# Optimization experiments

Measured on AMD Instinct MI355X. Metric: run time of the kernel, lower is better.

## Reference

```python
import jax, jax.numpy as jnp
import numpy as np

HEADS = 16
LN_EPS = 1e-5

def _ln(v, w, b):
    # LayerNorm over last dim (head dim s)
    mu = jnp.mean(v, axis=-1, keepdims=True)
    var = jnp.mean(jnp.square(v - mu), axis=-1, keepdims=True)
    return (v - mu) * jax.lax.rsqrt(var + LN_EPS) * w + b

def setup_inputs() -> dict:
    key = jax.random.key(0)
    ks = jax.random.split(key, 5)
    b, t, e = 2, 2048, 1024
    x = jax.random.normal(ks[0], (b, t, e), dtype=jnp.float32)
    scale = 0.02
    Wk = jax.random.normal(ks[1], (e, e), dtype=jnp.float32) * scale
    Wq = jax.random.normal(ks[2], (e, e), dtype=jnp.float32) * scale
    Wv = jax.random.normal(ks[3], (e, e), dtype=jnp.float32) * scale
    Wu = jax.random.normal(ks[4], (e, e), dtype=jnp.float32) * scale
    s = e // HEADS
    return {
        "x": x, "Wk": Wk, "Wq": Wq, "Wv": Wv, "Wu": Wu,
        "kln_w": jnp.ones((s,), jnp.float32), "kln_b": jnp.zeros((s,), jnp.float32),
        "qln_w": jnp.ones((s,), jnp.float32), "qln_b": jnp.zeros((s,), jnp.float32),
    }

def reference(x, Wk, Wq, Wv, Wu, kln_w, kln_b, qln_w, qln_b):
    b, t, e = x.shape
    h = HEADS
    s = e // h
    # nn.Linear: y = x @ W^T
    k = (x @ Wk.T).reshape(b, t, h, s)
    q = (x @ Wq.T).reshape(b, t, h, s)
    v = (x @ Wv.T).reshape(b, t, h, s)
    k = _ln(k, kln_w, kln_b)
    q = _ln(q, qln_w, qln_b)
    scalefactor = 1.0 / np.sqrt(s).astype(np.float32)
    # [b, h, t_q, t_k]
    dot = jnp.einsum('bqhs,bkhs->bhqk', q, k) * scalefactor
    causal = jnp.triu(jnp.ones((t, t), dtype=bool), k=1)  # mask strictly-upper (diag kept)
    dot = jnp.where(causal, -jnp.inf, dot)
    attn = jax.nn.softmax(dot, axis=-1)
    out = jnp.einsum('bhqk,bkhs->bqhs', attn, v).reshape(b, t, e)
    return out @ Wu.T
```

## Files before the change

### kernel.cpp

```cpp
#include <hip/hip_runtime.h>
#include <math.h>

#define T_SEQ 2048
#define E_DIM 1024
#define NH    16
#define HS    64
#define NB    2
#define M_ROWS 4096

typedef __attribute__((ext_vector_type(8))) short bf16x8;
typedef __attribute__((ext_vector_type(4))) short bf16x4;
typedef __attribute__((ext_vector_type(4))) float f32x4;

#define AS1 __attribute__((address_space(1)))
#define AS3 __attribute__((address_space(3)))

#define LOG2E 1.4426950408889634f

__device__ __forceinline__ f32x4 mfma16(bf16x4 a, bf16x4 b, f32x4 c) {
    return __builtin_amdgcn_mfma_f32_16x16x16bf16_1k(a, b, c, 0, 0, 0);
}

__device__ __forceinline__ ushort f2bf(float f) {
    union { float f; unsigned u; } c; c.f = f;
    unsigned r = c.u + 0x7fffu + ((c.u >> 16) & 1u);
    return (ushort)(r >> 16);
}
__device__ __forceinline__ ushort f2bf_trunc(float f) {
    union { float f; unsigned u; } c; c.f = f;
    return (ushort)(c.u >> 16);
}

__device__ __forceinline__ void load_lds16(const ushort* g, ushort* l) {
    __builtin_amdgcn_global_load_lds((const AS1 unsigned int*)g,
                                     (AS3 unsigned int*)l, 16, 0, 0);
}

__global__ __launch_bounds__(256) void cvt_all(
    const float* __restrict__ x,  const float* __restrict__ Wk,
    const float* __restrict__ Wq, const float* __restrict__ Wv,
    const float* __restrict__ Wu,
    ushort* __restrict__ xb,  ushort* __restrict__ Wkb,
    ushort* __restrict__ Wqb, ushort* __restrict__ Wvb,
    ushort* __restrict__ Wub)
{
    int i4 = blockIdx.x * 256 + threadIdx.x;
    int region = i4 >> 18;
    const float* src; ushort* dst; int off;
    if      (region < 4)  { src = x;  dst = xb;  off = i4; }
    else if (region == 4) { src = Wk; dst = Wkb; off = i4 - (4 << 18); }
    else if (region == 5) { src = Wq; dst = Wqb; off = i4 - (5 << 18); }
    else if (region == 6) { src = Wv; dst = Wvb; off = i4 - (6 << 18); }
    else                  { src = Wu; dst = Wub; off = i4 - (7 << 18); }
    float4 v = *(const float4*)(src + (size_t)off * 4);
    ushort4 o; o.x = f2bf(v.x); o.y = f2bf(v.y); o.z = f2bf(v.z); o.w = f2bf(v.w);
    *(ushort4*)(dst + (size_t)off * 4) = o;
}

__device__ __forceinline__ void gemm_core(
    const ushort* __restrict__ A, const ushort* __restrict__ W,
    int m0, int n0, ushort* As, ushort* Bs, f32x4 acc[4][4])
{
    const int tid  = threadIdx.x;
    const int lane = tid & 63, w = tid >> 6;
    const int quad = lane >> 4, l16 = lane & 15;
    const int wm = w & 1, wn = w >> 1;

    const int rl   = lane >> 2;
    const int gsw  = (lane & 3) ^ ((lane >> 3) & 3);
    const int fsw  = (l16 >> 1) & 3;

    const f32x4 zero = {0.f, 0.f, 0.f, 0.f};
#pragma unroll
    for (int mt = 0; mt < 4; ++mt)
#pragma unroll
        for (int nt = 0; nt < 4; ++nt) acc[mt][nt] = zero;

    for (int k0 = 0; k0 < E_DIM; k0 += 32) {
#pragma unroll
        for (int i = 0; i < 2; ++i) {
            int c = i * 4 + w;
            int row = c * 16 + rl;
            load_lds16(A + (size_t)(m0 + row) * E_DIM + k0 + gsw * 8, As + c * 512);
            load_lds16(W + (size_t)(n0 + row) * E_DIM + k0 + gsw * 8, Bs + c * 512);
        }
        __syncthreads();
        bf16x8 af[4], bfr[4];
#pragma unroll
        for (int mt = 0; mt < 4; ++mt)
            af[mt] = *(const bf16x8*)(As + (wm * 64 + mt * 16 + l16) * 32
                                      + ((quad ^ fsw) * 8));
#pragma unroll
        for (int nt = 0; nt < 4; ++nt)
            bfr[nt] = *(const bf16x8*)(Bs + (wn * 64 + nt * 16 + l16) * 32
                                       + ((quad ^ fsw) * 8));
#pragma unroll
        for (int mt = 0; mt < 4; ++mt)
#pragma unroll
            for (int nt = 0; nt < 4; ++nt)
                acc[mt][nt] = __builtin_amdgcn_mfma_f32_16x16x32_bf16(
                    af[mt], bfr[nt], acc[mt][nt], 0, 0, 0);
        __syncthreads();
    }
}

__global__ __launch_bounds__(256) void gemm_qkv(
    const ushort* __restrict__ A,
    const ushort* __restrict__ W0, const ushort* __restrict__ W1,
    const ushort* __restrict__ W2,
    ushort* __restrict__ Kb, ushort* __restrict__ Qb, ushort* __restrict__ Vt,
    const float* __restrict__ kw, const float* __restrict__ kbias,
    const float* __restrict__ qw, const float* __restrict__ qbias)
{
    __shared__ ushort As[128 * 32];
    __shared__ ushort Bs[128 * 32];
    const int z = blockIdx.z;
    const ushort* W = (z == 0) ? W0 : (z == 1) ? W1 : W2;
    const int m0 = blockIdx.y * 128, n0 = blockIdx.x * 128;
    f32x4 acc[4][4];
    gemm_core(A, W, m0, n0, As, Bs, acc);

    const int lane = threadIdx.x & 63, w = threadIdx.x >> 6;
    const int quad = lane >> 4, l16 = lane & 15;
    const int wm = w & 1, wn = w >> 1;
    const int row0 = m0 + wm * 64;
    const int col0 = n0 + wn * 64;

    if (z < 2) {
        ushort* C = z ? Qb : Kb;
        const float* lw = z ? qw : kw;
        const float* lb = z ? qbias : kbias;
        const float scale = z ? (0.125f * LOG2E) : 1.0f;
        float wv[4], bv_[4];
#pragma unroll
        for (int nt = 0; nt < 4; ++nt) {
            wv[nt]  = lw[nt * 16 + l16];
            bv_[nt] = lb[nt * 16 + l16];
        }
#pragma unroll
        for (int mt = 0; mt < 4; ++mt)
#pragma unroll
            for (int r = 0; r < 4; ++r) {
                float v[4], d[4];
#pragma unroll
                for (int nt = 0; nt < 4; ++nt) v[nt] = acc[mt][nt][r];
                float s = v[0] + v[1] + v[2] + v[3];
                s += __shfl_xor(s, 1); s += __shfl_xor(s, 2);
                s += __shfl_xor(s, 4); s += __shfl_xor(s, 8);
                float mu = s * (1.0f / 64.0f);
                float q2 = 0.f;
#pragma unroll
                for (int nt = 0; nt < 4; ++nt) { d[nt] = v[nt] - mu; q2 += d[nt] * d[nt]; }
                q2 += __shfl_xor(q2, 1); q2 += __shfl_xor(q2, 2);
                q2 += __shfl_xor(q2, 4); q2 += __shfl_xor(q2, 8);
                float rin = rsqrtf(q2 * (1.0f / 64.0f) + 1e-5f);
                int row = row0 + mt * 16 + quad * 4 + r;
#pragma unroll
                for (int nt = 0; nt < 4; ++nt)
                    C[(size_t)row * E_DIM + col0 + nt * 16 + l16] =
                        f2bf((d[nt] * rin * wv[nt] + bv_[nt]) * scale);
            }
    } else {
        const int bidx = m0 >> 11;
        const int hh   = col0 >> 6;
        const int t0   = (m0 & 2047) + wm * 64;
#pragma unroll
        for (int mt = 0; mt < 4; ++mt)
#pragma unroll
            for (int nt = 0; nt < 4; ++nt) {
                ushort4 pk = make_ushort4(f2bf(acc[mt][nt][0]), f2bf(acc[mt][nt][1]),
                                          f2bf(acc[mt][nt][2]), f2bf(acc[mt][nt][3]));
                size_t off = ((size_t)(bidx * NH + hh) * 64 + nt * 16 + l16) * T_SEQ
                             + t0 + mt * 16 + quad * 4;
                *(ushort4*)(Vt + off) = pk;
            }
    }
}

__global__ __launch_bounds__(256) void gemm_o(
    const ushort* __restrict__ A, const ushort* __restrict__ W,
    float* __restrict__ C)
{
    __shared__ ushort As[128 * 32];
    __shared__ ushort Bs[64 * 32];
    const int tid  = threadIdx.x;
    const int lane = tid & 63, w = tid >> 6;
    const int quad = lane >> 4, l16 = lane & 15;
    const int wm = w & 1, wn = w >> 1;
    const int m0 = blockIdx.y * 128, n0 = blockIdx.x * 64;

    const int rl  = lane >> 2;
    const int gsw = (lane & 3) ^ ((lane >> 3) & 3);
    const int fsw = (l16 >> 1) & 3;

    const f32x4 zero = {0.f, 0.f, 0.f, 0.f};
    f32x4 acc[4][2];
#pragma unroll
    for (int mt = 0; mt < 4; ++mt)
#pragma unroll
        for (int nt = 0; nt < 2; ++nt) acc[mt][nt] = zero;

    for (int k0 = 0; k0 < E_DIM; k0 += 32) {
#pragma unroll
        for (int i = 0; i < 2; ++i) {
            int c = i * 4 + w;
            int row = c * 16 + rl;
            load_lds16(A + (size_t)(m0 + row) * E_DIM + k0 + gsw * 8, As + c * 512);
        }
        {
            int row = w * 16 + rl;
            load_lds16(W + (size_t)(n0 + row) * E_DIM + k0 + gsw * 8, Bs + w * 512);
        }
        __syncthreads();
        bf16x8 af[4], bfr[2];
#pragma unroll
        for (int mt = 0; mt < 4; ++mt)
            af[mt] = *(const bf16x8*)(As + (wm * 64 + mt * 16 + l16) * 32
                                      + ((quad ^ fsw) * 8));
#pragma unroll
        for (int nt = 0; nt < 2; ++nt)
            bfr[nt] = *(const bf16x8*)(Bs + (wn * 32 + nt * 16 + l16) * 32
                                       + ((quad ^ fsw) * 8));
#pragma unroll
        for (int mt = 0; mt < 4; ++mt)
#pragma unroll
            for (int nt = 0; nt < 2; ++nt)
                acc[mt][nt] = __builtin_amdgcn_mfma_f32_16x16x32_bf16(
                    af[mt], bfr[nt], acc[mt][nt], 0, 0, 0);
        __syncthreads();
    }

    const int row0 = m0 + wm * 64;
    const int col0 = n0 + wn * 32;
#pragma unroll
    for (int mt = 0; mt < 4; ++mt)
#pragma unroll
        for (int nt = 0; nt < 2; ++nt)
#pragma unroll
            for (int r = 0; r < 4; ++r)
                C[(size_t)(row0 + mt * 16 + quad * 4 + r) * E_DIM
                  + col0 + nt * 16 + l16] = acc[mt][nt][r];
}

__global__ __launch_bounds__(256, 4) void flash_attn5(
    const ushort* __restrict__ Qg, const ushort* __restrict__ Kg,
    const ushort* __restrict__ Vt, ushort* __restrict__ O)
{
    __shared__ ushort Ks[2][64 * 64];
    __shared__ ushort Vs[2][64 * 64];

    const int tid  = threadIdx.x;
    const int lane = tid & 63, w = tid >> 6;
    const int quad = lane >> 4, l16 = lane & 15;

    const int L = blockIdx.x;
    const int c = L & 255, s = L >> 8;
    const int q0 = c >> 5;
    const int bh = c & 31;
    const int qt = (s == 0) ? q0 : (s == 1) ? (15 - q0)
                 : (s == 2) ? (16 + q0) : (31 - q0);
    const int b = bh >> 4, h = bh & 15;

    const ushort* Qbase = Qg + ((size_t)b * T_SEQ) * E_DIM + h * HS;
    const ushort* Kbase = Kg + ((size_t)b * T_SEQ) * E_DIM + h * HS;
    const ushort* Vbase = Vt + ((size_t)bh * HS) * T_SEQ;

    const int rloc = lane >> 3;
    const int gswc = (lane & 7) ^ rloc;
    const int sw   = l16 & 7;

    bf16x8 aq[2];
#pragma unroll
    for (int ks = 0; ks < 2; ++ks)
        aq[ks] = *(const bf16x8*)(Qbase + (size_t)(qt * 64 + w * 16 + l16) * E_DIM
                                  + ks * 32 + quad * 8);

    const f32x4 zero = {0.f, 0.f, 0.f, 0.f};
    f32x4 o_acc[4];
#pragma unroll
    for (int dt = 0; dt < 4; ++dt) o_acc[dt] = zero;
    float l_acc = 0.f;

#pragma unroll
    for (int i = 0; i < 2; ++i) {
        int cc = w * 2 + i, row = cc * 8 + rloc;
        load_lds16(Kbase + (size_t)row * E_DIM + gswc * 8, Ks[0] + cc * 512);
        load_lds16(Vbase + (size_t)row * T_SEQ + gswc * 8, Vs[0] + cc * 512);
    }

    const float M8 = 8.0f * LOG2E;

    for (int jt = 0; jt <= qt; ++jt) {
        const int buf = jt & 1;
        __syncthreads();
        if (jt < qt) {
#pragma unroll
            for (int i = 0; i < 2; ++i) {
                int cc = w * 2 + i, row = cc * 8 + rloc;
                load_lds16(Kbase + (size_t)(jt + 1) * 64 * E_DIM
                           + (size_t)row * E_DIM + gswc * 8, Ks[buf ^ 1] + cc * 512);
                load_lds16(Vbase + (size_t)row * T_SEQ + (jt + 1) * 64 + gswc * 8,
                           Vs[buf ^ 1] + cc * 512);
            }
        }

        f32x4 sa[4];
#pragma unroll
        for (int nt = 0; nt < 4; ++nt) sa[nt] = zero;
#pragma unroll
        for (int ks = 0; ks < 2; ++ks) {
            int cp = ((ks * 4 + quad) ^ sw) * 8;
#pragma unroll
            for (int nt = 0; nt < 4; ++nt) {
                bf16x8 bk = *(const bf16x8*)(Ks[buf] + (nt * 16 + l16) * 64 + cp);
                sa[nt] = __builtin_amdgcn_mfma_f32_16x16x32_bf16(bk, aq[ks], sa[nt], 0, 0, 0);
            }
        }

        if (jt == qt) {
#pragma unroll
            for (int nt = 0; nt < 4; ++nt)
#pragma unroll
                for (int r = 0; r < 4; ++r)
                    if (nt * 16 + quad * 4 + r > w * 16 + l16) sa[nt][r] = -1e30f;
        }

        bf16x4 bp[4];
#pragma unroll
        for (int nt = 0; nt < 4; ++nt)
#pragma unroll
            for (int r = 0; r < 4; ++r) {
                float p = __builtin_amdgcn_exp2f(sa[nt][r] - M8);
                l_acc += p;
                bp[nt][r] = (short)f2bf_trunc(p);
            }

#pragma unroll
        for (int kt = 0; kt < 4; ++kt) {
            const int tt = kt * 16 + quad * 4;
            const int ch = tt >> 3, el = tt & 7;
#pragma unroll
            for (int dt = 0; dt < 4; ++dt) {
                const int vd = dt * 16 + l16;
                bf16x4 va = *(const bf16x4*)(Vs[buf] + vd * 64
                                             + ((ch ^ (vd & 7)) << 3) + el);
                o_acc[dt] = mfma16(va, bp[kt], o_acc[dt]);
            }
        }
    }

    l_acc += __shfl_xor(l_acc, 16);
    l_acc += __shfl_xor(l_acc, 32);
    const float inv = 1.0f / l_acc;
    const int trow = qt * 64 + w * 16 + l16;
#pragma unroll
    for (int dt = 0; dt < 4; ++dt) {
        ushort4 pk = make_ushort4(f2bf(o_acc[dt][0] * inv), f2bf(o_acc[dt][1] * inv),
                                  f2bf(o_acc[dt][2] * inv), f2bf(o_acc[dt][3] * inv));
        *(ushort4*)(O + ((size_t)b * T_SEQ + trow) * E_DIM + h * HS
                    + dt * 16 + quad * 4) = pk;
    }
}

extern "C" void kernel_launch(void* const* d_in, const int* in_sizes, int n_in,
                              void* d_out, int out_size, void* d_ws, size_t ws_size,
                              hipStream_t stream) {
    const float* x     = (const float*)d_in[0];
    const float* Wk    = (const float*)d_in[1];
    const float* Wq    = (const float*)d_in[2];
    const float* Wv    = (const float*)d_in[3];
    const float* Wu    = (const float*)d_in[4];
    const float* kln_w = (const float*)d_in[5];
    const float* kln_b = (const float*)d_in[6];
    const float* qln_w = (const float*)d_in[7];
    const float* qln_b = (const float*)d_in[8];
    float* out = (float*)d_out;

    const size_t NE = (size_t)M_ROWS * E_DIM;
    const size_t NW = (size_t)E_DIM * E_DIM;
    ushort* xb  = (ushort*)d_ws;
    ushort* Wkb = xb  + NE;
    ushort* Wqb = Wkb + NW;
    ushort* Wvb = Wqb + NW;
    ushort* Wub = Wvb + NW;
    ushort* Kb  = Wub + NW;
    ushort* Qb  = Kb  + NE;
    ushort* Vt  = Qb  + NE;
    ushort* Ob  = Vt  + NE;

    cvt_all<<<8192, 256, 0, stream>>>(x, Wk, Wq, Wv, Wu, xb, Wkb, Wqb, Wvb, Wub);

    gemm_qkv<<<dim3(E_DIM / 128, M_ROWS / 128, 3), 256, 0, stream>>>(
        xb, Wkb, Wqb, Wvb, Kb, Qb, Vt, kln_w, kln_b, qln_w, qln_b);

    flash_attn5<<<1024, 256, 0, stream>>>(Qb, Kb, Vt, Ob);

    gemm_o<<<dim3(E_DIM / 64, M_ROWS / 128), 256, 0, stream>>>(Ob, Wub, out);
}
```

Before: 181.9 us.

## Double-buffer LDS tiles in GEMMs and enlarge output projection tiles

```diff
diff --git a/kernel.cpp b/kernel.cpp
--- a/kernel.cpp
+++ b/kernel.cpp
@@ -57,7 +57,7 @@
     *(ushort4*)(dst + (size_t)off * 4) = o;
 }
 
-__device__ __forceinline__ void gemm_core(
+__device__ __forceinline__ void gemm_core_db(
     const ushort* __restrict__ A, const ushort* __restrict__ W,
     int m0, int n0, ushort* As, ushort* Bs, f32x4 acc[4][4])
 {
@@ -76,23 +76,40 @@
 #pragma unroll
         for (int nt = 0; nt < 4; ++nt) acc[mt][nt] = zero;
 
+#pragma unroll
+    for (int i = 0; i < 2; ++i) {
+        int c = i * 4 + w;
+        int row = c * 16 + rl;
+        load_lds16(A + (size_t)(m0 + row) * E_DIM + gsw * 8, As + c * 512);
+        load_lds16(W + (size_t)(n0 + row) * E_DIM + gsw * 8, Bs + c * 512);
+    }
+
     for (int k0 = 0; k0 < E_DIM; k0 += 32) {
-#pragma unroll
-        for (int i = 0; i < 2; ++i) {
-            int c = i * 4 + w;
-            int row = c * 16 + rl;
-            load_lds16(A + (size_t)(m0 + row) * E_DIM + k0 + gsw * 8, As + c * 512);
-            load_lds16(W + (size_t)(n0 + row) * E_DIM + k0 + gsw * 8, Bs + c * 512);
-        }
+        const int buf = (k0 >> 5) & 1;
+        ushort* Ab = As + buf * 4096;
+        ushort* Bb = Bs + buf * 4096;
         __syncthreads();
+        if (k0 + 32 < E_DIM) {
+            ushort* An = As + (buf ^ 1) * 4096;
+            ushort* Bn = Bs + (buf ^ 1) * 4096;
+#pragma unroll
+            for (int i = 0; i < 2; ++i) {
+                int c = i * 4 + w;
+                int row = c * 16 + rl;
+                load_lds16(A + (size_t)(m0 + row) * E_DIM + k0 + 32 + gsw * 8,
+                           An + c * 512);
+                load_lds16(W + (size_t)(n0 + row) * E_DIM + k0 + 32 + gsw * 8,
+                           Bn + c * 512);
+            }
+        }
         bf16x8 af[4], bfr[4];
 #pragma unroll
         for (int mt = 0; mt < 4; ++mt)
-            af[mt] = *(const bf16x8*)(As + (wm * 64 + mt * 16 + l16) * 32
+            af[mt] = *(const bf16x8*)(Ab + (wm * 64 + mt * 16 + l16) * 32
                                       + ((quad ^ fsw) * 8));
 #pragma unroll
         for (int nt = 0; nt < 4; ++nt)
-            bfr[nt] = *(const bf16x8*)(Bs + (wn * 64 + nt * 16 + l16) * 32
+            bfr[nt] = *(const bf16x8*)(Bb + (wn * 64 + nt * 16 + l16) * 32
                                        + ((quad ^ fsw) * 8));
 #pragma unroll
         for (int mt = 0; mt < 4; ++mt)
@@ -100,7 +117,6 @@
             for (int nt = 0; nt < 4; ++nt)
                 acc[mt][nt] = __builtin_amdgcn_mfma_f32_16x16x32_bf16(
                     af[mt], bfr[nt], acc[mt][nt], 0, 0, 0);
-        __syncthreads();
     }
 }
 
@@ -112,13 +128,13 @@
     const float* __restrict__ kw, const float* __restrict__ kbias,
     const float* __restrict__ qw, const float* __restrict__ qbias)
 {
-    __shared__ ushort As[128 * 32];
-    __shared__ ushort Bs[128 * 32];
+    __shared__ ushort As[2 * 128 * 32];
+    __shared__ ushort Bs[2 * 128 * 32];
     const int z = blockIdx.z;
     const ushort* W = (z == 0) ? W0 : (z == 1) ? W1 : W2;
     const int m0 = blockIdx.y * 128, n0 = blockIdx.x * 128;
     f32x4 acc[4][4];
-    gemm_core(A, W, m0, n0, As, Bs, acc);
+    gemm_core_db(A, W, m0, n0, As, Bs, acc);
 
     const int lane = threadIdx.x & 63, w = threadIdx.x >> 6;
     const int quad = lane >> 4, l16 = lane & 15;
@@ -181,61 +197,20 @@
     const ushort* __restrict__ A, const ushort* __restrict__ W,
     float* __restrict__ C)
 {
-    __shared__ ushort As[128 * 32];
-    __shared__ ushort Bs[64 * 32];
-    const int tid  = threadIdx.x;
-    const int lane = tid & 63, w = tid >> 6;
+    __shared__ ushort As[2 * 128 * 32];
+    __shared__ ushort Bs[2 * 128 * 32];
+    const int m0 = blockIdx.y * 128, n0 = blockIdx.x * 128;
+    f32x4 acc[4][4];
+    gemm_core_db(A, W, m0, n0, As, Bs, acc);
+
+    const int lane = threadIdx.x & 63, w = threadIdx.x >> 6;
     const int quad = lane >> 4, l16 = lane & 15;
-    const int wm = w & 1, wn = w >> 1;
-    const int m0 = blockIdx.y * 128, n0 = blockIdx.x * 64;
-
-    const int rl  = lane >> 2;
-    const int gsw = (lane & 3) ^ ((lane >> 3) & 3);
-    const int fsw = (l16 >> 1) & 3;
-
-    const f32x4 zero = {0.f, 0.f, 0.f, 0.f};
-    f32x4 acc[4][2];
+    const int row0 = m0 + (w & 1) * 64;
+    const int col0 = n0 + (w >> 1) * 64;
 #pragma unroll
     for (int mt = 0; mt < 4; ++mt)
 #pragma unroll
-        for (int nt = 0; nt < 2; ++nt) acc[mt][nt] = zero;
-
-    for (int k0 = 0; k0 < E_DIM; k0 += 32) {
-#pragma unroll
-        for (int i = 0; i < 2; ++i) {
-            int c = i * 4 + w;
-            int row = c * 16 + rl;
-            load_lds16(A + (size_t)(m0 + row) * E_DIM + k0 + gsw * 8, As + c * 512);
-        }
-        {
-            int row = w * 16 + rl;
-            load_lds16(W + (size_t)(n0 + row) * E_DIM + k0 + gsw * 8, Bs + w * 512);
-        }
-        __syncthreads();
-        bf16x8 af[4], bfr[2];
-#pragma unroll
-        for (int mt = 0; mt < 4; ++mt)
-            af[mt] = *(const bf16x8*)(As + (wm * 64 + mt * 16 + l16) * 32
-                                      + ((quad ^ fsw) * 8));
-#pragma unroll
-        for (int nt = 0; nt < 2; ++nt)
-            bfr[nt] = *(const bf16x8*)(Bs + (wn * 32 + nt * 16 + l16) * 32
-                                       + ((quad ^ fsw) * 8));
-#pragma unroll
-        for (int mt = 0; mt < 4; ++mt)
-#pragma unroll
-            for (int nt = 0; nt < 2; ++nt)
-                acc[mt][nt] = __builtin_amdgcn_mfma_f32_16x16x32_bf16(
-                    af[mt], bfr[nt], acc[mt][nt], 0, 0, 0);
-        __syncthreads();
-    }
-
-    const int row0 = m0 + wm * 64;
-    const int col0 = n0 + wn * 32;
-#pragma unroll
-    for (int mt = 0; mt < 4; ++mt)
-#pragma unroll
-        for (int nt = 0; nt < 2; ++nt)
+        for (int nt = 0; nt < 4; ++nt)
 #pragma unroll
             for (int r = 0; r < 4; ++r)
                 C[(size_t)(row0 + mt * 16 + quad * 4 + r) * E_DIM
@@ -395,5 +370,5 @@
 
     flash_attn5<<<1024, 256, 0, stream>>>(Qb, Kb, Vt, Ob);
 
-    gemm_o<<<dim3(E_DIM / 64, M_ROWS / 128), 256, 0, stream>>>(Ob, Wub, out);
-}
+    gemm_o<<<dim3(E_DIM / 128, M_ROWS / 128), 256, 0, stream>>>(Ob, Wub, out);
+}
```

Result: no change. 181.5 us (-0.2%).
